# Optimization experiments

Measured on AMD Instinct MI355X. Metric: run time of the kernel, lower is better.

## Reference

```python
import jax, jax.numpy as jnp
import numpy as np

B, N, C_IN, C_OUT, E_DIM = 16, 1024, 64, 64, 4


def setup_inputs() -> dict:
    key = jax.random.key(0)
    ks = jax.random.split(key, 7)
    x = jax.random.normal(ks[0], (B, N, C_IN), dtype=jnp.float32)
    adj = jax.random.uniform(ks[1], (B, N, N), dtype=jnp.float32)
    edge_attr = jax.random.randint(ks[2], (B, N, N, 1), 0, E_DIM, dtype=jnp.int32)
    scale = 1.0 / np.sqrt(C_IN)
    W_rel = jax.random.normal(ks[3], (C_IN, C_OUT), dtype=jnp.float32) * scale
    b_rel = jax.random.normal(ks[4], (C_OUT,), dtype=jnp.float32) * scale
    W_root = jax.random.normal(ks[5], (C_IN, C_OUT), dtype=jnp.float32) * scale
    w_edge = jax.random.normal(ks[6], (E_DIM,), dtype=jnp.float32)
    return {"x": x, "adj": adj, "edge_attr": edge_attr,
            "W_rel": W_rel, "b_rel": b_rel, "W_root": W_root, "w_edge": w_edge}


def reference(x, adj, edge_attr, W_rel, b_rel, W_root, w_edge):
    # one_hot(edge_attr) @ w_edge == gather of w_edge by edge type (same math,
    # avoids materializing the B x N x N x E_DIM one-hot tensor).
    e = w_edge[edge_attr[..., 0]]            # [B, N, N]
    adj_w = adj * e                           # weighted adjacency
    out = jnp.matmul(adj_w, x)                # [B, N, C_IN] aggregation (aggr='add')
    out = jnp.matmul(out, W_rel) + b_rel      # lin_rel
    out = out + jnp.matmul(x, W_root)         # lin_root (no bias)
    return out
```

## Files before the change

### kernel.cpp

```cpp
#include <hip/hip_runtime.h>

#define BB 16
#define NN 1024
#define CC 64

typedef __attribute__((ext_vector_type(8))) short short8;
typedef __attribute__((ext_vector_type(4))) float f32x4;
typedef __attribute__((ext_vector_type(4))) int   i32x4;

typedef __attribute__((address_space(3))) void lds_void_t;
typedef const __attribute__((address_space(1))) void gbl_void_t;

__device__ __forceinline__ void load_lds16(const void* g, void* l) {
    __builtin_amdgcn_global_load_lds((gbl_void_t*)g, (lds_void_t*)l, 16, 0, 0);
}

__device__ __forceinline__ unsigned short bf16_rne(float f) {
    unsigned u = __float_as_uint(f);
    u += 0x7fffu + ((u >> 16) & 1u);
    return (unsigned short)(u >> 16);
}

extern "C" __global__ __launch_bounds__(256)
void precompute(const float* __restrict__ x, const float* __restrict__ W_rel,
                const float* __restrict__ W_root, const float* __restrict__ b_rel,
                unsigned short* __restrict__ xw_sw, float* __restrict__ out)
{
    __shared__ float wrel_s[64 * 64];
    __shared__ float wroot_s[64 * 64];
    __shared__ float x_s[16 * 68];

    const int t = threadIdx.x;
    #pragma unroll
    for (int k = 0; k < 4; ++k) {
        int i4 = t + 256 * k;
        ((float4*)wrel_s)[i4]  = ((const float4*)W_rel)[i4];
        ((float4*)wroot_s)[i4] = ((const float4*)W_root)[i4];
    }
    const int row0 = blockIdx.x * 16;
    {
        int r = t >> 4, c4 = t & 15;
        *(float4*)(x_s + r * 68 + c4 * 4) = ((const float4*)(x + (size_t)(row0 + r) * CC))[c4];
    }
    __syncthreads();

    const int c4 = t & 15;
    const int r  = t >> 4;
    float aw0 = 0.f, aw1 = 0.f, aw2 = 0.f, aw3 = 0.f;
    float ar0 = 0.f, ar1 = 0.f, ar2 = 0.f, ar3 = 0.f;
    const float* xrow = x_s + r * 68;
    #pragma unroll 8
    for (int k = 0; k < 64; ++k) {
        float xv = xrow[k];
        float4 wv = ((const float4*)(wrel_s  + k * 64))[c4];
        float4 rv = ((const float4*)(wroot_s + k * 64))[c4];
        aw0 += xv * wv.x; aw1 += xv * wv.y; aw2 += xv * wv.z; aw3 += xv * wv.w;
        ar0 += xv * rv.x; ar1 += xv * rv.y; ar2 += xv * rv.z; ar3 += xv * rv.w;
    }

    const int row_g = row0 + r;
    {
        const float4 bv = ((const float4*)b_rel)[c4];
        ((float4*)out)[(size_t)row_g * 16 + c4] =
            make_float4(ar0 + bv.x, ar1 + bv.y, ar2 + bv.z, ar3 + bv.w);
    }
    {
        const int b = row_g >> 10;
        const int k = row_g & 1023;
        const int kb = k >> 5;
        const int qk = (k >> 3) & 3;
        const int j  = k & 7;
        const int c  = 4 * c4;
        const int n0 = c >> 4;
        const int n  = c & 15;
        size_t off = ((size_t)b << 16) + (size_t)((kb * 4 + n0) << 9)
                   + (size_t)((n + (qk << 4)) << 3) + j;
        xw_sw[off]      = bf16_rne(aw0);
        xw_sw[off + 8]  = bf16_rne(aw1);
        xw_sw[off + 16] = bf16_rne(aw2);
        xw_sw[off + 24] = bf16_rne(aw3);
    }
}

extern "C" __global__ __launch_bounds__(256, 4)
void gnn_mfma(const float* __restrict__ adj, const int* __restrict__ ea,
              const float* __restrict__ w_edge,
              const unsigned short* __restrict__ xw_sw,
              float* __restrict__ out)
{
    __shared__ __align__(16) char lds[24576];

    const int t    = threadIdx.x;
    const int w    = t >> 6;
    const int lane = t & 63;
    const int m    = lane & 15;
    const int q    = lane >> 4;
    const int wm   = w >> 1;
    const int wn   = w & 1;

    const int mtile = blockIdx.x & 31;
    const int kh    = (blockIdx.x >> 5) & 1;
    const int b     = blockIdx.x >> 6;
    const int row0  = mtile << 5;

    const float w0 = w_edge[0], w1 = w_edge[1], w2 = w_edge[2], w3 = w_edge[3];
    const float d1 = w1 - w0;
    const float d2 = w2 - 2.f * w1 + w0;
    const float d3 = w3 - 3.f * w2 + 3.f * w1 - w0;
    const float c3 = d3 * (1.f / 6.f);
    const float c2 = 0.5f * d2 - 0.5f * d3;
    const float c1 = d1 - 0.5f * d2 + (1.f / 3.f) * d3;
    const float c0 = w0;

    const size_t bbase = ((size_t)b << 20);
    const int row_s = row0 + (wm << 4) + m;
    const int kbase = (kh << 9) + (q << 3) + (wn << 2);
    const float* adjp = adj + bbase + ((size_t)row_s << 10) + kbase;
    const int*   eap  = ea  + bbase + ((size_t)row_s << 10) + kbase;
    const int dA = (wm << 11) + (wn << 10);

    const unsigned short* xwp = xw_sw + ((size_t)b << 16)
                              + ((size_t)(((kh << 4) << 2) + (wn << 1)) << 9)
                              + ((size_t)lane << 3);

    f32x4 acc0 = {0.f, 0.f, 0.f, 0.f};
    f32x4 acc1 = acc0;
    short8 bfr[2][2];

#define WSEL(ev) __builtin_fmaf(__builtin_fmaf(__builtin_fmaf(c3, (float)(ev), c2), (float)(ev), c1), (float)(ev), c0)
#define BUFP(i) (lds + 8192 * (i))
#define STAGE(c, bi) do { \
        load_lds16(adjp + ((c) << 5), BUFP(bi) + dA); \
        load_lds16(eap  + ((c) << 5), BUFP(bi) + 4096 + dA); \
    } while (0)
#define LDBF(c, r) do { \
        bfr[r][0] = *(const short8*)(xwp + ((size_t)(c) << 11)); \
        bfr[r][1] = *(const short8*)(xwp + ((size_t)(c) << 11) + 512); \
    } while (0)
#define COMPUTE(bi, r) do { \
        const char* fb = BUFP(bi) + (wm << 11) + (lane << 4); \
        f32x4 alo = *(const f32x4*)(fb); \
        f32x4 ahi = *(const f32x4*)(fb + 1024); \
        i32x4 elo = *(const i32x4*)(fb + 4096); \
        i32x4 ehi = *(const i32x4*)(fb + 5120); \
        float p0 = alo[0] * WSEL(elo[0]); \
        float p1 = alo[1] * WSEL(elo[1]); \
        float p2 = alo[2] * WSEL(elo[2]); \
        float p3 = alo[3] * WSEL(elo[3]); \
        float p4 = ahi[0] * WSEL(ehi[0]); \
        float p5 = ahi[1] * WSEL(ehi[1]); \
        float p6 = ahi[2] * WSEL(ehi[2]); \
        float p7 = ahi[3] * WSEL(ehi[3]); \
        union { int i[4]; short8 s8; } af; \
        af.i[0] = __builtin_amdgcn_perm(__float_as_uint(p1), __float_as_uint(p0), 0x07060302u); \
        af.i[1] = __builtin_amdgcn_perm(__float_as_uint(p3), __float_as_uint(p2), 0x07060302u); \
        af.i[2] = __builtin_amdgcn_perm(__float_as_uint(p5), __float_as_uint(p4), 0x07060302u); \
        af.i[3] = __builtin_amdgcn_perm(__float_as_uint(p7), __float_as_uint(p6), 0x07060302u); \
        acc0 = __builtin_amdgcn_mfma_f32_16x16x32_bf16(af.s8, bfr[r][0], acc0, 0, 0, 0); \
        acc1 = __builtin_amdgcn_mfma_f32_16x16x32_bf16(af.s8, bfr[r][1], acc1, 0, 0, 0); \
    } while (0)

    STAGE(0, 0);
    LDBF(0, 0);

    #pragma unroll 16
    for (int c = 0; c < 16; ++c) {
        if (c < 15) {
            STAGE(c + 1, (c + 1) % 3);
            LDBF(c + 1, (c + 1) & 1);
            asm volatile("s_waitcnt vmcnt(4)" ::: "memory");
        } else {
            asm volatile("s_waitcnt vmcnt(0)" ::: "memory");
        }
        __builtin_amdgcn_s_barrier();
        COMPUTE(c % 3, c & 1);
    }

#undef COMPUTE
#undef LDBF
#undef STAGE
#undef BUFP
#undef WSEL

    float* ob = out + ((((size_t)b << 10) + row0 + (wm << 4) + (q << 2)) << 6)
              + (wn << 5) + m;
    #pragma unroll
    for (int rg = 0; rg < 4; ++rg) {
        atomicAdd(ob + rg * 64,      acc0[rg]);
        atomicAdd(ob + rg * 64 + 16, acc1[rg]);
    }
}

extern "C" void kernel_launch(void* const* d_in, const int* in_sizes, int n_in,
                              void* d_out, int out_size, void* d_ws, size_t ws_size,
                              hipStream_t stream) {
    const float* x      = (const float*)d_in[0];
    const float* adj    = (const float*)d_in[1];
    const int*   ea     = (const int*)  d_in[2];
    const float* W_rel  = (const float*)d_in[3];
    const float* b_rel  = (const float*)d_in[4];
    const float* W_root = (const float*)d_in[5];
    const float* w_edge = (const float*)d_in[6];
    float* out = (float*)d_out;

    unsigned short* xw_sw = (unsigned short*)d_ws;

    precompute<<<BB * NN / 16, 256, 0, stream>>>(x, W_rel, W_root, b_rel, xw_sw, out);
    gnn_mfma<<<BB * (NN / 32) * 2, 256, 0, stream>>>(adj, ea, w_edge, xw_sw, out);
}
```

Measured before the change: 171.8 us.

## Stage whole 32-row weighted adjacency tile in LDS as bf16, drop K-split

The K-split across two blocks is removed, so each block now covers all 1024 columns for 32 rows, and the atomics become plain read-modify-write adds. All threads first stream adj and edge types through registers with coalesced float4 loads, apply the edge weights, pack to bf16, and write a swizzled 64KB LDS tile. After one barrier, the MFMA loop reads A fragments from LDS and B from global. This removes the per-chunk barriers, the async LDS-copy pipeline and atomic contention. In exchange there is no overlap between the load phase and the MFMA phase, only half as many blocks, and lower occupancy because of the larger LDS footprint.

```diff
diff --git a/kernel.cpp b/kernel.cpp
--- a/kernel.cpp
+++ b/kernel.cpp
@@ -7,13 +7,6 @@
 typedef __attribute__((ext_vector_type(8))) short short8;
 typedef __attribute__((ext_vector_type(4))) float f32x4;
 typedef __attribute__((ext_vector_type(4))) int   i32x4;
-
-typedef __attribute__((address_space(3))) void lds_void_t;
-typedef const __attribute__((address_space(1))) void gbl_void_t;
-
-__device__ __forceinline__ void load_lds16(const void* g, void* l) {
-    __builtin_amdgcn_global_load_lds((gbl_void_t*)g, (lds_void_t*)l, 16, 0, 0);
-}
 
 __device__ __forceinline__ unsigned short bf16_rne(float f) {
     unsigned u = __float_as_uint(f);
@@ -82,25 +75,17 @@
     }
 }
 
-extern "C" __global__ __launch_bounds__(256, 4)
+extern "C" __global__ __launch_bounds__(256, 2)
 void gnn_mfma(const float* __restrict__ adj, const int* __restrict__ ea,
               const float* __restrict__ w_edge,
               const unsigned short* __restrict__ xw_sw,
               float* __restrict__ out)
 {
-    __shared__ __align__(16) char lds[24576];
+    __shared__ __align__(16) char lds[65536];
 
-    const int t    = threadIdx.x;
-    const int w    = t >> 6;
-    const int lane = t & 63;
-    const int m    = lane & 15;
-    const int q    = lane >> 4;
-    const int wm   = w >> 1;
-    const int wn   = w & 1;
-
+    const int t     = threadIdx.x;
     const int mtile = blockIdx.x & 31;
-    const int kh    = (blockIdx.x >> 5) & 1;
-    const int b     = blockIdx.x >> 6;
+    const int b     = blockIdx.x >> 5;
     const int row0  = mtile << 5;
 
     const float w0 = w_edge[0], w1 = w_edge[1], w2 = w_edge[2], w3 = w_edge[3];
@@ -112,82 +97,74 @@
     const float c1 = d1 - 0.5f * d2 + (1.f / 3.f) * d3;
     const float c0 = w0;
 
-    const size_t bbase = ((size_t)b << 20);
-    const int row_s = row0 + (wm << 4) + m;
-    const int kbase = (kh << 9) + (q << 3) + (wn << 2);
-    const float* adjp = adj + bbase + ((size_t)row_s << 10) + kbase;
-    const int*   eap  = ea  + bbase + ((size_t)row_s << 10) + kbase;
-    const int dA = (wm << 11) + (wn << 10);
+#define WSEL(ev) __builtin_fmaf(__builtin_fmaf(__builtin_fmaf(c3, (float)(ev), c2), (float)(ev), c1), (float)(ev), c0)
 
-    const unsigned short* xwp = xw_sw + ((size_t)b << 16)
-                              + ((size_t)(((kh << 4) << 2) + (wn << 1)) << 9)
-                              + ((size_t)lane << 3);
+    const size_t gbase = ((size_t)b << 20) + ((size_t)row0 << 10);
+    const float4* A4 = (const float4*)(adj + gbase);
+    const i32x4*  E4 = (const i32x4*)(ea + gbase);
+
+    const int kb_t   = t >> 3;
+    const int q_t    = (t >> 1) & 3;
+    const int X_t    = ((kb_t & 3) << 2) | q_t;
+    const int wbase  = (kb_t << 10) + (q_t << 8) + ((t & 1) << 3);
+
+    float4 aa[8]; i32x4 ee[8];
+    #pragma unroll
+    for (int d = 0; d < 8; ++d) { aa[d] = A4[d * 256 + t]; ee[d] = E4[d * 256 + t]; }
+
+    #pragma unroll
+    for (int i = 0; i < 32; ++i) {
+        float4 av = aa[i & 7];
+        i32x4  ev = ee[i & 7];
+        if (i < 24) {
+            aa[i & 7] = A4[(i + 8) * 256 + t];
+            ee[i & 7] = E4[(i + 8) * 256 + t];
+        }
+        float p0 = av.x * WSEL(ev[0]);
+        float p1 = av.y * WSEL(ev[1]);
+        float p2 = av.z * WSEL(ev[2]);
+        float p3 = av.w * WSEL(ev[3]);
+        unsigned u0 = __builtin_amdgcn_perm(__float_as_uint(p1), __float_as_uint(p0), 0x07060302u);
+        unsigned u1 = __builtin_amdgcn_perm(__float_as_uint(p3), __float_as_uint(p2), 0x07060302u);
+        const int m  = i & 15;
+        const int mh = i >> 4;
+        const int addr = (mh << 15) + wbase + ((m ^ X_t) << 4);
+        *(uint2*)(lds + addr) = make_uint2(u0, u1);
+    }
+    __syncthreads();
+
+    const int w    = t >> 6;
+    const int lane = t & 63;
+    const int m    = lane & 15;
+    const int q    = lane >> 4;
+    const int wm   = w >> 1;
+    const int wn   = w & 1;
+
+    const unsigned short* xwb = xw_sw + ((size_t)b << 16)
+                              + ((size_t)(wn * 2) << 9) + ((size_t)lane << 3);
+    const char* abase = lds + (wm << 15) + (q << 8);
 
     f32x4 acc0 = {0.f, 0.f, 0.f, 0.f};
     f32x4 acc1 = acc0;
-    short8 bfr[2][2];
 
-#define WSEL(ev) __builtin_fmaf(__builtin_fmaf(__builtin_fmaf(c3, (float)(ev), c2), (float)(ev), c1), (float)(ev), c0)
-#define BUFP(i) (lds + 8192 * (i))
-#define STAGE(c, bi) do { \
-        load_lds16(adjp + ((c) << 5), BUFP(bi) + dA); \
-        load_lds16(eap  + ((c) << 5), BUFP(bi) + 4096 + dA); \
-    } while (0)
-#define LDBF(c, r) do { \
-        bfr[r][0] = *(const short8*)(xwp + ((size_t)(c) << 11)); \
-        bfr[r][1] = *(const short8*)(xwp + ((size_t)(c) << 11) + 512); \
-    } while (0)
-#define COMPUTE(bi, r) do { \
-        const char* fb = BUFP(bi) + (wm << 11) + (lane << 4); \
-        f32x4 alo = *(const f32x4*)(fb); \
-        f32x4 ahi = *(const f32x4*)(fb + 1024); \
-        i32x4 elo = *(const i32x4*)(fb + 4096); \
-        i32x4 ehi = *(const i32x4*)(fb + 5120); \
-        float p0 = alo[0] * WSEL(elo[0]); \
-        float p1 = alo[1] * WSEL(elo[1]); \
-        float p2 = alo[2] * WSEL(elo[2]); \
-        float p3 = alo[3] * WSEL(elo[3]); \
-        float p4 = ahi[0] * WSEL(ehi[0]); \
-        float p5 = ahi[1] * WSEL(ehi[1]); \
-        float p6 = ahi[2] * WSEL(ehi[2]); \
-        float p7 = ahi[3] * WSEL(ehi[3]); \
-        union { int i[4]; short8 s8; } af; \
-        af.i[0] = __builtin_amdgcn_perm(__float_as_uint(p1), __float_as_uint(p0), 0x07060302u); \
-        af.i[1] = __builtin_amdgcn_perm(__float_as_uint(p3), __float_as_uint(p2), 0x07060302u); \
-        af.i[2] = __builtin_amdgcn_perm(__float_as_uint(p5), __float_as_uint(p4), 0x07060302u); \
-        af.i[3] = __builtin_amdgcn_perm(__float_as_uint(p7), __float_as_uint(p6), 0x07060302u); \
-        acc0 = __builtin_amdgcn_mfma_f32_16x16x32_bf16(af.s8, bfr[r][0], acc0, 0, 0, 0); \
-        acc1 = __builtin_amdgcn_mfma_f32_16x16x32_bf16(af.s8, bfr[r][1], acc1, 0, 0, 0); \
-    } while (0)
-
-    STAGE(0, 0);
-    LDBF(0, 0);
-
-    #pragma unroll 16
-    for (int c = 0; c < 16; ++c) {
-        if (c < 15) {
-            STAGE(c + 1, (c + 1) % 3);
-            LDBF(c + 1, (c + 1) & 1);
-            asm volatile("s_waitcnt vmcnt(4)" ::: "memory");
-        } else {
-            asm volatile("s_waitcnt vmcnt(0)" ::: "memory");
-        }
-        __builtin_amdgcn_s_barrier();
-        COMPUTE(c % 3, c & 1);
+    #pragma unroll
+    for (int kb = 0; kb < 32; ++kb) {
+        const int X = ((kb & 3) << 2) | q;
+        short8 af = *(const short8*)(abase + (kb << 10) + ((m ^ X) << 4));
+        const unsigned short* xq = xwb + ((size_t)kb << 11);
+        short8 bf0 = *(const short8*)(xq);
+        short8 bf1 = *(const short8*)(xq + 512);
+        acc0 = __builtin_amdgcn_mfma_f32_16x16x32_bf16(af, bf0, acc0, 0, 0, 0);
+        acc1 = __builtin_amdgcn_mfma_f32_16x16x32_bf16(af, bf1, acc1, 0, 0, 0);
     }
-
-#undef COMPUTE
-#undef LDBF
-#undef STAGE
-#undef BUFP
 #undef WSEL
 
-    float* ob = out + ((((size_t)b << 10) + row0 + (wm << 4) + (q << 2)) << 6)
-              + (wn << 5) + m;
+    const size_t R0 = ((size_t)b << 10) + row0 + (wm << 4) + (q << 2);
+    float* ob = out + (R0 << 6) + (wn << 5) + m;
     #pragma unroll
     for (int rg = 0; rg < 4; ++rg) {
-        atomicAdd(ob + rg * 64,      acc0[rg]);
-        atomicAdd(ob + rg * 64 + 16, acc1[rg]);
+        ob[rg * 64]      += acc0[rg];
+        ob[rg * 64 + 16] += acc1[rg];
     }
 }
 
@@ -206,5 +183,5 @@
     unsigned short* xw_sw = (unsigned short*)d_ws;
 
     precompute<<<BB * NN / 16, 256, 0, stream>>>(x, W_rel, W_root, b_rel, xw_sw, out);
-    gnn_mfma<<<BB * (NN / 32) * 2, 256, 0, stream>>>(adj, ea, w_edge, xw_sw, out);
+    gnn_mfma<<<BB * (NN / 32), 256, 0, stream>>>(adj, ea, w_edge, xw_sw, out);
 }
```

After: 173.8 us. Within noise of the previous version (+1.1%).
